# Kernel tuning notes

Hardware: AMD Instinct MI355X
Metric: run time of the kernel (lower is better)

The kernel has to match this reference:

```python
import jax, jax.numpy as jnp
import numpy as np

B, N, D_IN, D_OUT, H = 4, 512, 1024, 1024, 16
HD = D_IN // H      # key head dim (FAISS k_features)
VD = D_OUT // H     # value head dim
MEM = 32768         # memory_size per head
IPQ = 8             # items_per_query
SCALE = HD ** -0.5


def setup_inputs() -> dict:
    key = jax.random.key(0)
    ks = jax.random.split(key, 9)
    s = 0.02
    return {
        "x": jax.random.normal(ks[0], (B, N, D_IN), jnp.float32),
        "Wq": jax.random.normal(ks[1], (D_IN, D_IN), jnp.float32) * s,
        "Wk": jax.random.normal(ks[2], (D_IN, D_IN), jnp.float32) * s,
        "Wv": jax.random.normal(ks[3], (D_OUT, D_IN), jnp.float32) * s,
        "Ww": jax.random.normal(ks[4], (D_OUT, D_IN), jnp.float32) * s,
        "Wo": jax.random.normal(ks[5], (D_OUT, D_OUT), jnp.float32) * s,
        "bo": jnp.zeros((D_OUT,), jnp.float32),
        "k_mem0": jax.random.normal(ks[6], (H, MEM, HD), jnp.float32) * s,
        "v_mem0": jax.random.normal(ks[7], (H, MEM, VD), jnp.float32) * s,
    }


def _attention(q, k, v, Wo, bo):
    # q: [b,n,D_IN], k: [b,m,D_IN], v: [b,m,D_OUT]
    b, n, _ = q.shape
    m = k.shape[1]
    qh = q.reshape(b, n, H, HD)
    kh = k.reshape(b, m, H, HD)
    vh = v.reshape(b, m, H, VD)
    sim = jnp.einsum("bihd,bjhd->bhij", qh, kh) * SCALE
    att = jax.nn.softmax(sim, axis=-1)
    out = jnp.einsum("bhij,bjhd->bihd", att, vh).reshape(b, n, H * VD)
    return out @ Wo.T + bo


def reference(x, Wq, Wk, Wv, Ww, Wo, bo, k_mem0, v_mem0):
    b, n, _ = x.shape
    q = x @ Wq.T          # [b,n,D_IN]
    k = x @ Wk.T          # [b,n,D_IN]
    v = x @ Wv.T          # [b,n,D_OUT]
    w = jax.nn.sigmoid(x @ Ww.T)

    a = _attention(q, k, v, Wo, bo)

    # per-head flat views: [h, b*n, hd]
    qh = q.reshape(b, n, H, HD).transpose(2, 0, 1, 3).reshape(H, b * n, HD)
    kh = k.reshape(b, n, H, HD).transpose(2, 0, 1, 3).reshape(H, b * n, HD)
    vh = v.reshape(b, n, H, VD).transpose(2, 0, 1, 3).reshape(H, b * n, VD)

    m_ins = b * n
    # FIFO insert: drop oldest m_ins rows, append new keys/values
    k_mem = jnp.concatenate([k_mem0[:, m_ins:], kh], axis=1)  # [h, MEM, HD]
    v_mem = jnp.concatenate([v_mem0[:, m_ins:], vh], axis=1)  # [h, MEM, VD]

    # exact inner-product search (IndexFlatIP), top IPQ per query, per head
    sims = jnp.einsum("hqd,hmd->hqm", qh, k_mem)               # [h, b*n, MEM]
    _, idx = jax.lax.top_k(sims, IPQ)                          # [h, b*n, IPQ]
    idx = idx.reshape(H, b * n * IPQ, 1)
    k_ret = jnp.take_along_axis(k_mem, idx, axis=1)            # [h, b*n*IPQ, HD]
    v_ret = jnp.take_along_axis(v_mem, idx, axis=1)            # [h, b*n*IPQ, VD]

    # 'h (b m) hd -> b m (h hd)' with m = n*IPQ
    k_m = k_ret.reshape(H, b, n * IPQ, HD).transpose(1, 2, 0, 3).reshape(b, n * IPQ, D_IN)
    v_m = v_ret.reshape(H, b, n * IPQ, VD).transpose(1, 2, 0, 3).reshape(b, n * IPQ, D_OUT)

    a_m = _attention(q, k_m, v_m, Wo, bo)
    return w * a + (1.0 - w) * a_m
```

## Files before the change

kernel.cpp:

```cpp
#include <hip/hip_runtime.h>
#include <float.h>
#include <math.h>


#define DIN   1024
#define NHEADS 16
#define HD    64
#define NB    4
#define NSEQ  512
#define BN    2048
#define MEMN  32768
#define OLDN  30720
#define IPQ   8
#define ATT_SCALE 0.125f
#define SZ    (BN * DIN)

typedef __attribute__((ext_vector_type(4))) float floatx4;
typedef __attribute__((ext_vector_type(8))) short short8;

__device__ __forceinline__ unsigned short f2bf(float f) {
    unsigned int u = __float_as_uint(f);
    return (unsigned short)((u + 0x7FFFu + ((u >> 16) & 1u)) >> 16);
}
__device__ __forceinline__ float bf2f(unsigned short s) {
    return __uint_as_float(((unsigned int)s) << 16);
}
__device__ __forceinline__ void split_pack(float4 a, float4 b, short8 &hi, short8 &lo) {
    float vals[8] = {a.x, a.y, a.z, a.w, b.x, b.y, b.z, b.w};
#pragma unroll
    for (int j = 0; j < 8; ++j) {
        unsigned short h = f2bf(vals[j]);
        hi[j] = (short)h;
        lo[j] = (short)f2bf(vals[j] - bf2f(h));
    }
}
__device__ __forceinline__ floatx4 mfma16(short8 a, short8 b, floatx4 c) {
    return __builtin_amdgcn_mfma_f32_16x16x32_bf16(a, b, c, 0, 0, 0);
}

__global__ void init_kernel(unsigned int* nrm) {
    if (threadIdx.x < NHEADS) nrm[threadIdx.x] = 0u;
}

__global__ __launch_bounds__(256) void gemm_mfma(
    const float* __restrict__ A,
    const float* __restrict__ W0, const float* __restrict__ W1,
    const float* __restrict__ W2, const float* __restrict__ W3,
    float* __restrict__ C0, float* __restrict__ C1,
    float* __restrict__ C2, float* __restrict__ C3,
    int sigmoidZ)
{
    __shared__ short Ahi_s[128 * 32];
    __shared__ short Alo_s[128 * 32];
    __shared__ short Bhi_s[128 * 32];
    __shared__ short Blo_s[128 * 32];

    int z = blockIdx.z;
    const float* W = (z == 0) ? W0 : (z == 1) ? W1 : (z == 2) ? W2 : W3;
    float* C = (z == 0) ? C0 : (z == 1) ? C1 : (z == 2) ? C2 : C3;

    int tid = threadIdx.x;
    int wv = tid >> 6, lane = tid & 63, quad = lane >> 4, l16 = lane & 15;
    int row0 = blockIdx.y * 128, col0 = blockIdx.x * 128;
    int wm = (wv >> 1) * 64, wn = (wv & 1) * 64;

    floatx4 zero4 = {0.f, 0.f, 0.f, 0.f};
    floatx4 acc[4][4];
#pragma unroll
    for (int i = 0; i < 4; ++i)
#pragma unroll
        for (int j = 0; j < 4; ++j) acc[i][j] = zero4;

    for (int kk = 0; kk < DIN; kk += 32) {
        __syncthreads();
#pragma unroll
        for (int p = 0; p < 2; ++p) {
            int g = tid * 2 + p;
            int row = g >> 2, cc = (g & 3) * 8;
            const float* ap = A + (size_t)(row0 + row) * DIN + kk + cc;
            float4 a0 = *(const float4*)ap;
            float4 a1 = *(const float4*)(ap + 4);
            short8 h8, l8;
            split_pack(a0, a1, h8, l8);
            *(short8*)&Ahi_s[g * 8] = h8;
            *(short8*)&Alo_s[g * 8] = l8;
            const float* bp = W + (size_t)(col0 + row) * DIN + kk + cc;
            float4 b0 = *(const float4*)bp;
            float4 b1 = *(const float4*)(bp + 4);
            split_pack(b0, b1, h8, l8);
            *(short8*)&Bhi_s[g * 8] = h8;
            *(short8*)&Blo_s[g * 8] = l8;
        }
        __syncthreads();

        short8 ah[4], al[4], bh[4], bl[4];
#pragma unroll
        for (int t = 0; t < 4; ++t) {
            int ar = (wm + t * 16 + l16) * 32 + quad * 8;
            int br = (wn + t * 16 + l16) * 32 + quad * 8;
            ah[t] = *(const short8*)&Ahi_s[ar];
            al[t] = *(const short8*)&Alo_s[ar];
            bh[t] = *(const short8*)&Bhi_s[br];
            bl[t] = *(const short8*)&Blo_s[br];
        }
#pragma unroll
        for (int tm = 0; tm < 4; ++tm)
#pragma unroll
            for (int tn = 0; tn < 4; ++tn) {
                floatx4 c = acc[tm][tn];
                c = mfma16(al[tm], bl[tn], c);
                c = mfma16(al[tm], bh[tn], c);
                c = mfma16(ah[tm], bl[tn], c);
                c = mfma16(ah[tm], bh[tn], c);
                acc[tm][tn] = c;
            }
    }

    bool sig = (sigmoidZ == z);
#pragma unroll
    for (int tm = 0; tm < 4; ++tm)
#pragma unroll
        for (int tn = 0; tn < 4; ++tn)
#pragma unroll
            for (int r = 0; r < 4; ++r) {
                int row = row0 + wm + tm * 16 + quad * 4 + r;
                int col = col0 + wn + tn * 16 + l16;
                float vv = acc[tm][tn][r];
                if (sig) vv = 1.f / (1.f + __expf(-vv));
                C[(size_t)row * DIN + col] = vv;
            }
}

__global__ __launch_bounds__(256) void oldnorm_kernel(
    const float* __restrict__ kmem0, unsigned int* __restrict__ nrm)
{
    int h = blockIdx.y;
    int c0 = blockIdx.x * 1024;
    int part = threadIdx.x & 15, rg = threadIdx.x >> 4;
    const float* base = kmem0 + ((size_t)h * MEMN + BN) * HD;
    float mx = 0.f;
    for (int it = 0; it < 64; ++it) {
        int row = c0 + it * 16 + rg;
        float4 vv = *(const float4*)(base + (size_t)row * HD + part * 4);
        float s = vv.x * vv.x + vv.y * vv.y + vv.z * vv.z + vv.w * vv.w;
#pragma unroll
        for (int o = 1; o < 16; o <<= 1) s += __shfl_xor(s, o, 16);
        mx = fmaxf(mx, s);
    }
    __shared__ float red[256];
    red[threadIdx.x] = mx;
    __syncthreads();
    for (int st = 128; st > 0; st >>= 1) {
        if (threadIdx.x < st) red[threadIdx.x] = fmaxf(red[threadIdx.x], red[threadIdx.x + st]);
        __syncthreads();
    }
    if (threadIdx.x == 0) atomicMax(nrm + h, __float_as_uint(sqrtf(red[0])));
}

__device__ __forceinline__ void insert_top8(float (&tv)[8], int (&ti)[8], float v, int id) {
    if (v < tv[7] || (v == tv[7] && id > ti[7])) return;
    tv[7] = v; ti[7] = id;
#pragma unroll
    for (int s = 7; s > 0; --s) {
        bool sw = (tv[s] > tv[s - 1]) || (tv[s] == tv[s - 1] && ti[s] < ti[s - 1]);
        if (sw) {
            float fv = tv[s]; tv[s] = tv[s - 1]; tv[s - 1] = fv;
            int iv = ti[s]; ti[s] = ti[s - 1]; ti[s - 1] = iv;
        }
    }
}

__global__ __launch_bounds__(256, 2) void search_kernel(
    const float* __restrict__ q, const float* __restrict__ knew,
    const float* __restrict__ kmem0, const unsigned int* __restrict__ nrm,
    int* __restrict__ idxOut)
{
    __shared__ short Khi[32 * 72];
    __shared__ short Klo[32 * 72];
    __shared__ int sflag;
    int tid = threadIdx.x;
    int qt = blockIdx.x, h = blockIdx.y;
    int wv = tid >> 6, lane = tid & 63, quad = lane >> 4, l16 = lane & 15;
    if (tid == 0) sflag = 0;

    short8 qhi[2], qlo[2];
    float qn2;
    {
        int qrow = qt * 64 + wv * 16 + l16;
        const float* qp = q + (size_t)qrow * DIN + h * HD;
        float sq = 0.f;
#pragma unroll
        for (int st = 0; st < 2; ++st) {
            float4 a = *(const float4*)(qp + st * 32 + quad * 8);
            float4 c = *(const float4*)(qp + st * 32 + quad * 8 + 4);
            sq += a.x * a.x + a.y * a.y + a.z * a.z + a.w * a.w
                + c.x * c.x + c.y * c.y + c.z * c.z + c.w * c.w;
            split_pack(a, c, qhi[st], qlo[st]);
        }
        sq += __shfl_xor(sq, 16);
        sq += __shfl_xor(sq, 32);
        qn2 = sq;
    }

    float tv[4][8]; int ti[4][8];
#pragma unroll
    for (int r = 0; r < 4; ++r)
#pragma unroll
        for (int s = 0; s < 8; ++s) { tv[r][s] = -FLT_MAX; ti[r][s] = 0x7FFFFFFF; }

    for (int ch = 0; ch < 64; ++ch) {
        __syncthreads();
        {
            int key = tid >> 3, part = tid & 7;
            const float* kr = knew + (size_t)(ch * 32 + key) * DIN + h * HD;
            float4 ka = *(const float4*)(kr + part * 8);
            float4 kb = *(const float4*)(kr + part * 8 + 4);
            short8 kh8, kl8;
            split_pack(ka, kb, kh8, kl8);
            *(short8*)&Khi[key * 72 + part * 8] = kh8;
            *(short8*)&Klo[key * 72 + part * 8] = kl8;
        }
        __syncthreads();

        short8 kh00 = *(const short8*)&Khi[l16 * 72 + quad * 8];
        short8 kh01 = *(const short8*)&Khi[l16 * 72 + 32 + quad * 8];
        short8 kl00 = *(const short8*)&Klo[l16 * 72 + quad * 8];
        short8 kl01 = *(const short8*)&Klo[l16 * 72 + 32 + quad * 8];
        short8 kh10 = *(const short8*)&Khi[(16 + l16) * 72 + quad * 8];
        short8 kh11 = *(const short8*)&Khi[(16 + l16) * 72 + 32 + quad * 8];
        short8 kl10 = *(const short8*)&Klo[(16 + l16) * 72 + quad * 8];
        short8 kl11 = *(const short8*)&Klo[(16 + l16) * 72 + 32 + quad * 8];
        floatx4 zero4 = {0.f, 0.f, 0.f, 0.f};
        floatx4 s0 = zero4, s1 = zero4;
        s0 = mfma16(qhi[0], kh00, s0); s0 = mfma16(qhi[1], kh01, s0);
        s0 = mfma16(qlo[0], kh00, s0); s0 = mfma16(qlo[1], kh01, s0);
        s0 = mfma16(qhi[0], kl00, s0); s0 = mfma16(qhi[1], kl01, s0);
        s1 = mfma16(qhi[0], kh10, s1); s1 = mfma16(qhi[1], kh11, s1);
        s1 = mfma16(qlo[0], kh10, s1); s1 = mfma16(qlo[1], kh11, s1);
        s1 = mfma16(qhi[0], kl10, s1); s1 = mfma16(qhi[1], kl11, s1);

        int base = OLDN + ch * 32;
#pragma unroll
        for (int r = 0; r < 4; ++r) {
            insert_top8(tv[r], ti[r], s0[r], base + l16);
            insert_top8(tv[r], ti[r], s1[r], base + 16 + l16);
        }
    }

    float val8[4], keepv[4];
    int keepi[4];
#pragma unroll
    for (int rr = 0; rr < 4; ++rr) { keepv[rr] = -FLT_MAX; keepi[rr] = 0x7FFFFFFF; val8[rr] = -FLT_MAX; }
#pragma unroll
    for (int rr = 0; rr < 4; ++rr) {
#pragma unroll
        for (int m = 0; m < 8; ++m) {
            float cv = tv[rr][0]; int ci = ti[rr][0];
#pragma unroll
            for (int o = 1; o < 16; o <<= 1) {
                float ov = __shfl_xor(cv, o, 16);
                int oi = __shfl_xor(ci, o, 16);
                if (ov > cv || (ov == cv && oi < ci)) { cv = ov; ci = oi; }
            }
            if (tv[rr][0] == cv && ti[rr][0] == ci) {
#pragma unroll
                for (int s = 0; s < 7; ++s) { tv[rr][s] = tv[rr][s + 1]; ti[rr][s] = ti[rr][s + 1]; }
                tv[rr][7] = -FLT_MAX; ti[rr][7] = 0x7FFFFFFF;
            }
            if (l16 == m) { keepv[rr] = cv; keepi[rr] = ci; }
            if (l16 == 0)
                idxOut[((size_t)h * BN + qt * 64 + wv * 16 + quad * 4 + rr) * IPQ + m] = ci;
            val8[rr] = cv;
        }
    }

    float oldMax = __uint_as_float(nrm[h]);
    bool need = false;
#pragma unroll
    for (int rr = 0; rr < 4; ++rr) {
        float bq = __shfl(qn2, quad * 4 + rr, 16);
        float bnd = sqrtf(bq) * oldMax * 1.0001f + 1e-5f;
        if (bnd >= val8[rr]) need = true;
    }
    if (need) sflag = 1;
    __syncthreads();

    if (sflag) {
#pragma unroll
        for (int rr = 0; rr < 4; ++rr) {
            tv[rr][0] = (l16 < 8) ? keepv[rr] : -FLT_MAX;
            ti[rr][0] = (l16 < 8) ? keepi[rr] : 0x7FFFFFFF;
#pragma unroll
            for (int s = 1; s < 8; ++s) { tv[rr][s] = -FLT_MAX; ti[rr][s] = 0x7FFFFFFF; }
        }
        for (int ch = 0; ch < 960; ++ch) {
            __syncthreads();
            {
                int key = tid >> 3, part = tid & 7;
                const float* kr = kmem0 + ((size_t)h * MEMN + BN + ch * 32 + key) * HD;
                float4 ka = *(const float4*)(kr + part * 8);
                float4 kb = *(const float4*)(kr + part * 8 + 4);
                short8 kh8, kl8;
                split_pack(ka, kb, kh8, kl8);
                *(short8*)&Khi[key * 72 + part * 8] = kh8;
                *(short8*)&Klo[key * 72 + part * 8] = kl8;
            }
            __syncthreads();

            short8 kh00 = *(const short8*)&Khi[l16 * 72 + quad * 8];
            short8 kh01 = *(const short8*)&Khi[l16 * 72 + 32 + quad * 8];
            short8 kl00 = *(const short8*)&Klo[l16 * 72 + quad * 8];
            short8 kl01 = *(const short8*)&Klo[l16 * 72 + 32 + quad * 8];
            short8 kh10 = *(const short8*)&Khi[(16 + l16) * 72 + quad * 8];
            short8 kh11 = *(const short8*)&Khi[(16 + l16) * 72 + 32 + quad * 8];
            short8 kl10 = *(const short8*)&Klo[(16 + l16) * 72 + quad * 8];
            short8 kl11 = *(const short8*)&Klo[(16 + l16) * 72 + 32 + quad * 8];
            floatx4 zero4 = {0.f, 0.f, 0.f, 0.f};
            floatx4 s0 = zero4, s1 = zero4;
            s0 = mfma16(qhi[0], kh00, s0); s0 = mfma16(qhi[1], kh01, s0);
            s0 = mfma16(qlo[0], kh00, s0); s0 = mfma16(qlo[1], kh01, s0);
            s0 = mfma16(qhi[0], kl00, s0); s0 = mfma16(qhi[1], kl01, s0);
            s1 = mfma16(qhi[0], kh10, s1); s1 = mfma16(qhi[1], kh11, s1);
            s1 = mfma16(qlo[0], kh10, s1); s1 = mfma16(qlo[1], kh11, s1);
            s1 = mfma16(qhi[0], kl10, s1); s1 = mfma16(qhi[1], kl11, s1);

            int base = ch * 32;
#pragma unroll
            for (int r = 0; r < 4; ++r) {
                insert_top8(tv[r], ti[r], s0[r], base + l16);
                insert_top8(tv[r], ti[r], s1[r], base + 16 + l16);
            }
        }
#pragma unroll
        for (int rr = 0; rr < 4; ++rr) {
#pragma unroll
            for (int m = 0; m < 8; ++m) {
                float cv = tv[rr][0]; int ci = ti[rr][0];
#pragma unroll
                for (int o = 1; o < 16; o <<= 1) {
                    float ov = __shfl_xor(cv, o, 16);
                    int oi = __shfl_xor(ci, o, 16);
                    if (ov > cv || (ov == cv && oi < ci)) { cv = ov; ci = oi; }
                }
                if (tv[rr][0] == cv && ti[rr][0] == ci) {
#pragma unroll
                    for (int s = 0; s < 7; ++s) { tv[rr][s] = tv[rr][s + 1]; ti[rr][s] = ti[rr][s + 1]; }
                    tv[rr][7] = -FLT_MAX; ti[rr][7] = 0x7FFFFFFF;
                }
                if (l16 == 0)
                    idxOut[((size_t)h * BN + qt * 64 + wv * 16 + quad * 4 + rr) * IPQ + m] = ci;
            }
        }
    }
}

__global__ __launch_bounds__(256, 2) void attn_kernel(
    const float* __restrict__ q, const float* __restrict__ knew,
    const float* __restrict__ vnew, const float* __restrict__ kmem0,
    const float* __restrict__ vmem0, const int* __restrict__ idxb,
    float* __restrict__ outp, int gatherMode, int nkeys)
{
    __shared__ short Khi[32 * 72];
    __shared__ short Klo[32 * 72];
    __shared__ short Vthi[64 * 40];
    __shared__ short Vtlo[64 * 40];
    __shared__ short Pbuf[4 * 16 * 40];
    int tid = threadIdx.x;
    int pair = blockIdx.x, qt = blockIdx.y;
    int h = pair >> 2, b = pair & 3;
    int wv = tid >> 6, lane = tid & 63, quad = lane >> 4, l16 = lane & 15;

    short8 qhi[2], qlo[2];
    {
        int qrow = b * NSEQ + qt * 64 + wv * 16 + l16;
        const float* qp = q + (size_t)qrow * DIN + h * HD;
#pragma unroll
        for (int st = 0; st < 2; ++st) {
            float4 a = *(const float4*)(qp + st * 32 + quad * 8);
            float4 c = *(const float4*)(qp + st * 32 + quad * 8 + 4);
            split_pack(a, c, qhi[st], qlo[st]);
        }
    }
    floatx4 zero4 = {0.f, 0.f, 0.f, 0.f};
    floatx4 Oacc[4];
#pragma unroll
    for (int t = 0; t < 4; ++t) Oacc[t] = zero4;
    float mrow[4], lrow[4];
#pragma unroll
    for (int r = 0; r < 4; ++r) { mrow[r] = -3.0e38f; lrow[r] = 0.f; }

    int key = tid >> 3, part = tid & 7;
    int vcol = (((key >> 3) ^ (part & 3)) << 3) | (key & 7);
    float4 ka, kb, va, vb;
    auto gload = [&](int chl) {
        const float *kr, *vr;
        if (!gatherMode) {
            int row = b * NSEQ + chl * 32 + key;
            kr = knew + (size_t)row * DIN + h * HD;
            vr = vnew + (size_t)row * DIN + h * HD;
        } else {
            int J = chl * 32 + key;
            int mi = idxb[((size_t)h * BN + b * NSEQ + (J >> 3)) * IPQ + (J & 7)];
            if (mi < OLDN) {
                kr = kmem0 + ((size_t)h * MEMN + BN + mi) * HD;
                vr = vmem0 + ((size_t)h * MEMN + BN + mi) * HD;
            } else {
                kr = knew + (size_t)(mi - OLDN) * DIN + h * HD;
                vr = vnew + (size_t)(mi - OLDN) * DIN + h * HD;
            }
        }
        ka = *(const float4*)(kr + part * 8);
        kb = *(const float4*)(kr + part * 8 + 4);
        va = *(const float4*)(vr + part * 8);
        vb = *(const float4*)(vr + part * 8 + 4);
    };

    int nch = nkeys >> 5;
    gload(0);
    for (int ch = 0; ch < nch; ++ch) {
        asm volatile("s_waitcnt lgkmcnt(0)" ::: "memory");
        __builtin_amdgcn_s_barrier();

        {
            short8 kh8, kl8;
            split_pack(ka, kb, kh8, kl8);
            *(short8*)&Khi[key * 72 + part * 8] = kh8;
            *(short8*)&Klo[key * 72 + part * 8] = kl8;
            float vals[8] = {va.x, va.y, va.z, va.w, vb.x, vb.y, vb.z, vb.w};
#pragma unroll
            for (int u = 0; u < 8; ++u) {
                int d = part * 8 + u;
                unsigned short hh = f2bf(vals[u]);
                Vthi[d * 40 + vcol] = (short)hh;
                Vtlo[d * 40 + vcol] = (short)f2bf(vals[u] - bf2f(hh));
            }
        }
        if (ch + 1 < nch) gload(ch + 1);

        asm volatile("s_waitcnt lgkmcnt(0)" ::: "memory");
        __builtin_amdgcn_s_barrier();

        short8 kh00 = *(const short8*)&Khi[(l16) * 72 + 0 * 32 + quad * 8];
        short8 kh01 = *(const short8*)&Khi[(l16) * 72 + 1 * 32 + quad * 8];
        short8 kl00 = *(const short8*)&Klo[(l16) * 72 + 0 * 32 + quad * 8];
        short8 kl01 = *(const short8*)&Klo[(l16) * 72 + 1 * 32 + quad * 8];
        short8 kh10 = *(const short8*)&Khi[(16 + l16) * 72 + 0 * 32 + quad * 8];
        short8 kh11 = *(const short8*)&Khi[(16 + l16) * 72 + 1 * 32 + quad * 8];
        short8 kl10 = *(const short8*)&Klo[(16 + l16) * 72 + 0 * 32 + quad * 8];
        short8 kl11 = *(const short8*)&Klo[(16 + l16) * 72 + 1 * 32 + quad * 8];
        floatx4 s0 = zero4, s1 = zero4;
        s0 = mfma16(qhi[0], kh00, s0); s0 = mfma16(qhi[1], kh01, s0);
        s0 = mfma16(qlo[0], kh00, s0); s0 = mfma16(qlo[1], kh01, s0);
        s0 = mfma16(qhi[0], kl00, s0); s0 = mfma16(qhi[1], kl01, s0);
        s1 = mfma16(qhi[0], kh10, s1); s1 = mfma16(qhi[1], kh11, s1);
        s1 = mfma16(qlo[0], kh10, s1); s1 = mfma16(qlo[1], kh11, s1);
        s1 = mfma16(qhi[0], kl10, s1); s1 = mfma16(qhi[1], kl11, s1);

        float cm[4], alpha[4], p0[4], p1[4], rs[4];
#pragma unroll
        for (int r = 0; r < 4; ++r) cm[r] = fmaxf(s0[r], s1[r]) * ATT_SCALE;
#pragma unroll
        for (int o = 1; o < 16; o <<= 1) {
#pragma unroll
            for (int r = 0; r < 4; ++r) cm[r] = fmaxf(cm[r], __shfl_xor(cm[r], o, 16));
        }
#pragma unroll
        for (int r = 0; r < 4; ++r) {
            float mn = fmaxf(mrow[r], cm[r]);
            alpha[r] = __expf(mrow[r] - mn);
            p0[r] = __expf(s0[r] * ATT_SCALE - mn);
            p1[r] = __expf(s1[r] * ATT_SCALE - mn);
            mrow[r] = mn;
            rs[r] = p0[r] + p1[r];
        }
#pragma unroll
        for (int o = 1; o < 16; o <<= 1) {
#pragma unroll
            for (int r = 0; r < 4; ++r) rs[r] += __shfl_xor(rs[r], o, 16);
        }
#pragma unroll
        for (int r = 0; r < 4; ++r) {
            lrow[r] = lrow[r] * alpha[r] + rs[r];
            Pbuf[(wv * 16 + quad * 4 + r) * 40 + l16] = (short)f2bf(p0[r]);
            Pbuf[(wv * 16 + quad * 4 + r) * 40 + 16 + l16] = (short)f2bf(p1[r]);
        }
#pragma unroll
        for (int t = 0; t < 4; ++t)
#pragma unroll
            for (int r = 0; r < 4; ++r) Oacc[t][r] *= alpha[r];

        short8 pf = *(const short8*)&Pbuf[(wv * 16 + l16) * 40 + quad * 8];
#pragma unroll
        for (int t = 0; t < 4; ++t) {
            int dd = t * 16 + l16;
            int vc = ((quad ^ ((dd >> 3) & 3)) << 3);
            short8 vh = *(const short8*)&Vthi[dd * 40 + vc];
            short8 vl = *(const short8*)&Vtlo[dd * 40 + vc];
            floatx4 o = Oacc[t];
            o = mfma16(pf, vh, o);
            o = mfma16(pf, vl, o);
            Oacc[t] = o;
        }
    }
#pragma unroll
    for (int t = 0; t < 4; ++t)
#pragma unroll
        for (int r = 0; r < 4; ++r) {
            int qrow = b * NSEQ + qt * 64 + wv * 16 + quad * 4 + r;
            outp[(size_t)qrow * DIN + h * HD + t * 16 + l16] = Oacc[t][r] / lrow[r];
        }
}

__global__ __launch_bounds__(256) void combine_kernel(
    const float* __restrict__ G, const float* __restrict__ wg,
    const float* __restrict__ bo, float* __restrict__ out)
{
    int gid = blockIdx.x * 256 + threadIdx.x;
    float4 g1 = ((const float4*)G)[gid];
    float4 g2 = ((const float4*)G)[gid + (SZ / 4)];
    float4 w4 = ((const float4*)wg)[gid];
    float4 b4 = ((const float4*)bo)[gid & (DIN / 4 - 1)];
    float4 o;
    o.x = w4.x * g1.x + (1.f - w4.x) * g2.x + b4.x;
    o.y = w4.y * g1.y + (1.f - w4.y) * g2.y + b4.y;
    o.z = w4.z * g1.z + (1.f - w4.z) * g2.z + b4.z;
    o.w = w4.w * g1.w + (1.f - w4.w) * g2.w + b4.w;
    ((float4*)out)[gid] = o;
}

extern "C" void kernel_launch(void* const* d_in, const int* in_sizes, int n_in,
                              void* d_out, int out_size, void* d_ws, size_t ws_size,
                              hipStream_t stream)
{
    (void)in_sizes; (void)n_in; (void)out_size; (void)ws_size;
    const float* x     = (const float*)d_in[0];
    const float* Wq    = (const float*)d_in[1];
    const float* Wk    = (const float*)d_in[2];
    const float* Wv    = (const float*)d_in[3];
    const float* Ww    = (const float*)d_in[4];
    const float* Wo    = (const float*)d_in[5];
    const float* bo    = (const float*)d_in[6];
    const float* kmem0 = (const float*)d_in[7];
    const float* vmem0 = (const float*)d_in[8];

    float* ws = (float*)d_ws;
    float* q  = ws;
    float* k  = ws + (size_t)SZ;
    float* v  = ws + (size_t)2 * SZ;
    float* wg = ws + (size_t)3 * SZ;
    float* AO = ws + (size_t)4 * SZ;
    float* G  = ws + (size_t)6 * SZ;
    int* idxb = (int*)(ws + (size_t)8 * SZ);
    unsigned int* nrm = (unsigned int*)(ws + (size_t)8 * SZ + NHEADS * BN * IPQ);

    init_kernel<<<1, 64, 0, stream>>>(nrm);
    gemm_mfma<<<dim3(8, 16, 4), 256, 0, stream>>>(x, Wq, Wk, Wv, Ww, q, k, v, wg, 3);
    oldnorm_kernel<<<dim3(30, 16), 256, 0, stream>>>(kmem0, nrm);
    search_kernel<<<dim3(32, 16), 256, 0, stream>>>(q, k, kmem0, nrm, idxb);
    attn_kernel<<<dim3(64, 8, 1), 256, 0, stream>>>(q, k, v, kmem0, vmem0, idxb, AO, 0, 512);
    attn_kernel<<<dim3(64, 8, 1), 256, 0, stream>>>(q, k, v, kmem0, vmem0, idxb,
                                                    AO + (size_t)SZ, 1, 4096);
    gemm_mfma<<<dim3(8, 32, 1), 256, 0, stream>>>(AO, Wo, Wo, Wo, Wo, G, G, G, G, -1);
    combine_kernel<<<2048, 256, 0, stream>>>(G, wg, bo, (float*)d_out);
}
```

Before: 998.3 us.

## Merge attention launches with split-K memory attention and packed bf16 conversion

The two attention launches are merged into one grid where blockIdx.y selects local attention or one of two halves of the 4096-key memory attention. The split halves write unnormalized outputs plus row max and sum, and a new combine2 kernel merges them with log-sum-exp rescaling. This gives the long memory pass more parallelism and lets it overlap with the short local pass. It also swaps scalar bf16 rounding for the packed v_cvt_pk_bf16_f32 instruction and changes V loads to strided scalar loads that are stored transposed without the XOR swizzle, which may add LDS bank conflicts and uncoalesced global reads.

```diff
diff --git a/kernel.cpp b/kernel.cpp
--- a/kernel.cpp
+++ b/kernel.cpp
@@ -25,14 +25,23 @@
 __device__ __forceinline__ float bf2f(unsigned short s) {
     return __uint_as_float(((unsigned int)s) << 16);
 }
+__device__ __forceinline__ unsigned cvt_pk_bf16(float a, float b) {
+    unsigned r;
+    asm("v_cvt_pk_bf16_f32 %0, %1, %2" : "=v"(r) : "v"(a), "v"(b));
+    return r;
+}
 __device__ __forceinline__ void split_pack(float4 a, float4 b, short8 &hi, short8 &lo) {
-    float vals[8] = {a.x, a.y, a.z, a.w, b.x, b.y, b.z, b.w};
-#pragma unroll
-    for (int j = 0; j < 8; ++j) {
-        unsigned short h = f2bf(vals[j]);
-        hi[j] = (short)h;
-        lo[j] = (short)f2bf(vals[j] - bf2f(h));
-    }
+    float v[8] = {a.x, a.y, a.z, a.w, b.x, b.y, b.z, b.w};
+    union { unsigned u[4]; short8 s; } H, L;
+#pragma unroll
+    for (int j = 0; j < 4; ++j) {
+        unsigned h = cvt_pk_bf16(v[2 * j], v[2 * j + 1]);
+        float r0 = v[2 * j]     - __uint_as_float(h << 16);
+        float r1 = v[2 * j + 1] - __uint_as_float(h & 0xFFFF0000u);
+        H.u[j] = h;
+        L.u[j] = cvt_pk_bf16(r0, r1);
+    }
+    hi = H.s; lo = L.s;
 }
 __device__ __forceinline__ floatx4 mfma16(short8 a, short8 b, floatx4 c) {
     return __builtin_amdgcn_mfma_f32_16x16x32_bf16(a, b, c, 0, 0, 0);
@@ -358,7 +367,7 @@
     const float* __restrict__ q, const float* __restrict__ knew,
     const float* __restrict__ vnew, const float* __restrict__ kmem0,
     const float* __restrict__ vmem0, const int* __restrict__ idxb,
-    float* __restrict__ outp, int gatherMode, int nkeys)
+    float* __restrict__ AO, float* __restrict__ G)
 {
     __shared__ short Khi[32 * 72];
     __shared__ short Klo[32 * 72];
@@ -366,7 +375,7 @@
     __shared__ short Vtlo[64 * 40];
     __shared__ short Pbuf[4 * 16 * 40];
     int tid = threadIdx.x;
-    int pair = blockIdx.x, qt = blockIdx.y;
+    int pair = blockIdx.x, mode = blockIdx.y, qt = blockIdx.z;
     int h = pair >> 2, b = pair & 3;
     int wv = tid >> 6, lane = tid & 63, quad = lane >> 4, l16 = lane & 15;
 
@@ -390,11 +399,11 @@
     for (int r = 0; r < 4; ++r) { mrow[r] = -3.0e38f; lrow[r] = 0.f; }
 
     int key = tid >> 3, part = tid & 7;
-    int vcol = (((key >> 3) ^ (part & 3)) << 3) | (key & 7);
-    float4 ka, kb, va, vb;
+    float4 ka, kb;
+    float vv[8];
     auto gload = [&](int chl) {
         const float *kr, *vr;
-        if (!gatherMode) {
+        if (mode == 0) {
             int row = b * NSEQ + chl * 32 + key;
             kr = knew + (size_t)row * DIN + h * HD;
             vr = vnew + (size_t)row * DIN + h * HD;
@@ -411,13 +420,14 @@
         }
         ka = *(const float4*)(kr + part * 8);
         kb = *(const float4*)(kr + part * 8 + 4);
-        va = *(const float4*)(vr + part * 8);
-        vb = *(const float4*)(vr + part * 8 + 4);
+#pragma unroll
+        for (int u = 0; u < 8; ++u) vv[u] = vr[part + 8 * u];
     };
 
-    int nch = nkeys >> 5;
-    gload(0);
-    for (int ch = 0; ch < nch; ++ch) {
+    int ch0 = (mode == 2) ? 64 : 0;
+    int ch1 = (mode == 0) ? 16 : ((mode == 1) ? 64 : 128);
+    gload(ch0);
+    for (int ch = ch0; ch < ch1; ++ch) {
         asm volatile("s_waitcnt lgkmcnt(0)" ::: "memory");
         __builtin_amdgcn_s_barrier();
 
@@ -426,16 +436,19 @@
             split_pack(ka, kb, kh8, kl8);
             *(short8*)&Khi[key * 72 + part * 8] = kh8;
             *(short8*)&Klo[key * 72 + part * 8] = kl8;
-            float vals[8] = {va.x, va.y, va.z, va.w, vb.x, vb.y, vb.z, vb.w};
-#pragma unroll
-            for (int u = 0; u < 8; ++u) {
-                int d = part * 8 + u;
-                unsigned short hh = f2bf(vals[u]);
-                Vthi[d * 40 + vcol] = (short)hh;
-                Vtlo[d * 40 + vcol] = (short)f2bf(vals[u] - bf2f(hh));
-            }
-        }
-        if (ch + 1 < nch) gload(ch + 1);
+#pragma unroll
+            for (int u = 0; u < 8; u += 2) {
+                unsigned hh = cvt_pk_bf16(vv[u], vv[u + 1]);
+                float r0 = vv[u]     - __uint_as_float(hh << 16);
+                float r1 = vv[u + 1] - __uint_as_float(hh & 0xFFFF0000u);
+                unsigned ll = cvt_pk_bf16(r0, r1);
+                Vthi[(part + 8 * u) * 40 + key]       = (short)(hh & 0xFFFF);
+                Vthi[(part + 8 * (u + 1)) * 40 + key] = (short)(hh >> 16);
+                Vtlo[(part + 8 * u) * 40 + key]       = (short)(ll & 0xFFFF);
+                Vtlo[(part + 8 * (u + 1)) * 40 + key] = (short)(ll >> 16);
+            }
+        }
+        if (ch + 1 < ch1) gload(ch + 1);
 
         asm volatile("s_waitcnt lgkmcnt(0)" ::: "memory");
         __builtin_amdgcn_s_barrier();
@@ -481,8 +494,9 @@
 #pragma unroll
         for (int r = 0; r < 4; ++r) {
             lrow[r] = lrow[r] * alpha[r] + rs[r];
-            Pbuf[(wv * 16 + quad * 4 + r) * 40 + l16] = (short)f2bf(p0[r]);
-            Pbuf[(wv * 16 + quad * 4 + r) * 40 + 16 + l16] = (short)f2bf(p1[r]);
+            unsigned pw = cvt_pk_bf16(p0[r], p1[r]);
+            Pbuf[(wv * 16 + quad * 4 + r) * 40 + l16]      = (short)(pw & 0xFFFF);
+            Pbuf[(wv * 16 + quad * 4 + r) * 40 + 16 + l16] = (short)(pw >> 16);
         }
 #pragma unroll
         for (int t = 0; t < 4; ++t)
@@ -492,23 +506,63 @@
         short8 pf = *(const short8*)&Pbuf[(wv * 16 + l16) * 40 + quad * 8];
 #pragma unroll
         for (int t = 0; t < 4; ++t) {
-            int dd = t * 16 + l16;
-            int vc = ((quad ^ ((dd >> 3) & 3)) << 3);
-            short8 vh = *(const short8*)&Vthi[dd * 40 + vc];
-            short8 vl = *(const short8*)&Vtlo[dd * 40 + vc];
+            short8 vh = *(const short8*)&Vthi[(t * 16 + l16) * 40 + quad * 8];
+            short8 vl = *(const short8*)&Vtlo[(t * 16 + l16) * 40 + quad * 8];
             floatx4 o = Oacc[t];
             o = mfma16(pf, vh, o);
             o = mfma16(pf, vl, o);
             Oacc[t] = o;
         }
     }
-#pragma unroll
-    for (int t = 0; t < 4; ++t)
-#pragma unroll
-        for (int r = 0; r < 4; ++r) {
-            int qrow = b * NSEQ + qt * 64 + wv * 16 + quad * 4 + r;
-            outp[(size_t)qrow * DIN + h * HD + t * 16 + l16] = Oacc[t][r] / lrow[r];
-        }
+    if (mode == 0) {
+#pragma unroll
+        for (int t = 0; t < 4; ++t)
+#pragma unroll
+            for (int r = 0; r < 4; ++r) {
+                int qrow = b * NSEQ + qt * 64 + wv * 16 + quad * 4 + r;
+                AO[(size_t)qrow * DIN + h * HD + t * 16 + l16] = Oacc[t][r] / lrow[r];
+            }
+    } else {
+        float* ob = (mode == 1) ? (AO + (size_t)SZ) : G;
+        float* mlbuf = G + (size_t)SZ + ((size_t)(mode - 1) * NHEADS + h) * BN * 2;
+#pragma unroll
+        for (int t = 0; t < 4; ++t)
+#pragma unroll
+            for (int r = 0; r < 4; ++r) {
+                int qrow = b * NSEQ + qt * 64 + wv * 16 + quad * 4 + r;
+                ob[(size_t)qrow * DIN + h * HD + t * 16 + l16] = Oacc[t][r];
+            }
+        if (l16 == 0) {
+#pragma unroll
+            for (int r = 0; r < 4; ++r) {
+                int qrow = b * NSEQ + qt * 64 + wv * 16 + quad * 4 + r;
+                float2 mlv = {mrow[r], lrow[r]};
+                *(float2*)&mlbuf[(size_t)qrow * 2] = mlv;
+            }
+        }
+    }
+}
+
+__global__ __launch_bounds__(256) void combine2_kernel(
+    float* __restrict__ O0, const float* __restrict__ O1,
+    const float* __restrict__ ml)
+{
+    int g = blockIdx.x * 256 + threadIdx.x;
+    int row = g >> 8;
+    int h = (g >> 4) & 15;
+    float2 ml0 = *(const float2*)&ml[((size_t)h * BN + row) * 2];
+    float2 ml1 = *(const float2*)&ml[(((size_t)NHEADS + h) * BN + row) * 2];
+    float m = fmaxf(ml0.x, ml1.x);
+    float a0 = __expf(ml0.x - m), a1 = __expf(ml1.x - m);
+    float inv = 1.f / (ml0.y * a0 + ml1.y * a1);
+    float4 o0 = ((const float4*)O0)[g];
+    float4 o1 = ((const float4*)O1)[g];
+    float4 o;
+    o.x = (o0.x * a0 + o1.x * a1) * inv;
+    o.y = (o0.y * a0 + o1.y * a1) * inv;
+    o.z = (o0.z * a0 + o1.z * a1) * inv;
+    o.w = (o0.w * a0 + o1.w * a1) * inv;
+    ((float4*)O0)[g] = o;
 }
 
 __global__ __launch_bounds__(256) void combine_kernel(
@@ -557,9 +611,8 @@
     gemm_mfma<<<dim3(8, 16, 4), 256, 0, stream>>>(x, Wq, Wk, Wv, Ww, q, k, v, wg, 3);
     oldnorm_kernel<<<dim3(30, 16), 256, 0, stream>>>(kmem0, nrm);
     search_kernel<<<dim3(32, 16), 256, 0, stream>>>(q, k, kmem0, nrm, idxb);
-    attn_kernel<<<dim3(64, 8, 1), 256, 0, stream>>>(q, k, v, kmem0, vmem0, idxb, AO, 0, 512);
-    attn_kernel<<<dim3(64, 8, 1), 256, 0, stream>>>(q, k, v, kmem0, vmem0, idxb,
-                                                    AO + (size_t)SZ, 1, 4096);
+    attn_kernel<<<dim3(64, 3, 8), 256, 0, stream>>>(q, k, v, kmem0, vmem0, idxb, AO, G);
+    combine2_kernel<<<2048, 256, 0, stream>>>(AO + (size_t)SZ, G, G + (size_t)SZ);
     gemm_mfma<<<dim3(8, 32, 1), 256, 0, stream>>>(AO, Wo, Wo, Wo, Wo, G, G, G, G, -1);
     combine_kernel<<<2048, 256, 0, stream>>>(G, wg, bo, (float*)d_out);
 }
```

Measured after the change: 982.5 us. No clear change (-1.6%).
